# Kernel tuning notes

Measured on AMD Instinct MI355X. Metric: run time of the kernel, lower is better.

Reference implementation:

```python
import jax, jax.numpy as jnp
import numpy as np

LOSS_W = 0.6
UNC_W = 0.4
EPS = 1e-8


def setup_inputs() -> dict:
    key = jax.random.key(0)
    ks = jax.random.split(key, 6)
    B, D, C, BANK = 1024, 256, 80, 65536
    return {
        "features": jax.random.normal(ks[0], (B, D), jnp.float32),
        "predictions": jax.random.normal(ks[1], (B, C), jnp.float32),
        "targets": jax.random.uniform(ks[2], (B, C), dtype=jnp.float32),
        "query": jax.random.normal(ks[3], (B, D), jnp.float32),
        "memory": jax.random.normal(ks[4], (BANK, D), jnp.float32),
        "importance_scores": jax.random.uniform(ks[5], (BANK,), dtype=jnp.float32),
        "index": BANK,  # bank pre-filled (steady state)
        "k": 8,
    }


def _difficulty(predictions, targets):
    # per-sample BCE-with-logits, mean over classes
    bce = -(targets * jax.nn.log_sigmoid(predictions)
            + (1.0 - targets) * jax.nn.log_sigmoid(-predictions))
    sl = bce.mean(axis=1)                                   # [B]
    mx = sl.max()
    sl = jnp.where(mx > 0, sl / (mx + EPS), sl)
    probs = jax.nn.sigmoid(predictions)
    confidence = jnp.abs(probs - 0.5).mean(axis=1)
    uncertainty = jnp.clip(1.0 - 2.0 * confidence, 0.0, 1.0)
    return LOSS_W * sl + UNC_W * uncertainty                # [B]


def _update(memory, importance_scores, index, features, difficulty):
    # 'hard' mode: store samples above the 0.7 difficulty quantile,
    # sequential priority (min-replacement) insertion via scan.
    bank_size = memory.shape[0]
    thr = jnp.quantile(difficulty, 0.7)
    store = difficulty > thr                                # [B] bool

    def step(carry, inp):
        mem, scores, idx = carry
        feat, score, st = inp
        fill = idx < bank_size
        min_idx = jnp.argmin(scores)
        min_score = scores[min_idx]
        widx = jnp.where(fill, idx, min_idx)
        do_write = st & (fill | (score > min_score))
        mem = mem.at[widx].set(jnp.where(do_write, feat, mem[widx]))
        scores = scores.at[widx].set(jnp.where(do_write, score, scores[widx]))
        idx = idx + jnp.where(st & fill, 1, 0).astype(idx.dtype)
        return (mem, scores, idx), None

    init = (memory, importance_scores, jnp.asarray(index, jnp.int32))
    (mem, scores, idx), _ = jax.lax.scan(step, init, (features, difficulty, store))
    return mem, scores, idx


def _l2norm(x):
    # torch F.normalize: x / max(||x||, eps)
    n = jnp.linalg.norm(x, axis=1, keepdims=True)
    return x / jnp.maximum(n, 1e-12)


def reference(features, predictions, targets, query, memory, importance_scores, index, k):
    difficulty = _difficulty(predictions, targets)
    mem, scores, idx = _update(memory, importance_scores, index, features, difficulty)
    # retrieve: bank is full (index starts at bank_size) -> valid_size == bank_size
    sim = _l2norm(query) @ _l2norm(mem).T                   # [B, BANK]
    w, ind = jax.lax.top_k(sim, k)                          # [B, k]
    weights = jax.nn.softmax(w, axis=1)                     # [B, k]
    gathered = mem[ind]                                     # [B, k, D]
    return jnp.einsum('bk,bkd->bd', weights, gathered)      # [B, D]
```

## Files before the change

kernel.cpp:

```cpp
#include <hip/hip_runtime.h>
#include <hip/hip_bf16.h>
#include <stdint.h>

#define BANK 65536
#define BQ 1024
#define DIM 256
#define NCLS 80
#define KTOP 8
#define CAND_CAP 1024
#define SCORE_CUT 0.007f
#define NSPLIT 128
#define SPLIT_ROWS 512
#define NT 16
#define TAU 0.2f
#define SCAP 96

typedef __attribute__((ext_vector_type(8))) short short8;
typedef __attribute__((ext_vector_type(4))) float f32x4;

__device__ __forceinline__ unsigned int mono_f32(float f) {
    unsigned int b = __float_as_uint(f);
    return (b & 0x80000000u) ? ~b : (b | 0x80000000u);
}
__device__ __forceinline__ float unmono_f32(unsigned int u) {
    unsigned int b = (u & 0x80000000u) ? (u & 0x7FFFFFFFu) : ~u;
    return __uint_as_float(b);
}
__device__ __forceinline__ unsigned short f2bf(float f) {
    unsigned int u = __float_as_uint(f);
    unsigned int r = ((u >> 16) & 1u) + 0x7FFFu;
    return (unsigned short)((u + r) >> 16);
}
__device__ __forceinline__ void stage16(const char* gsrc, char* ldst) {
    __builtin_amdgcn_global_load_lds(
        (const __attribute__((address_space(1))) unsigned int*)gsrc,
        (__attribute__((address_space(3))) unsigned int*)ldst, 16, 0, 0);
}

#define INS8(L, key) do { \
    _Pragma("unroll") \
    for (int pp = 7; pp >= 1; --pp) { \
        unsigned long long prev = L[pp - 1]; \
        L[pp] = (L[pp] >= (key)) ? L[pp] : ((prev >= (key)) ? (key) : prev); \
    } \
    L[0] = (L[0] >= (key)) ? L[0] : (key); \
} while (0)

__global__ void prep_all(const float* __restrict__ memory, const float* __restrict__ features,
                         const float* __restrict__ query,
                         const float* __restrict__ pred, const float* __restrict__ targ,
                         const float* __restrict__ scores,
                         unsigned short* __restrict__ Mn, unsigned short* __restrict__ Qn,
                         float* __restrict__ invm, float* __restrict__ invq,
                         float* __restrict__ sl_raw, float* __restrict__ unc,
                         int* __restrict__ ovw, unsigned long long* __restrict__ cand,
                         int* __restrict__ meta) {
    int bx = blockIdx.x;
    if (bx < 16640) {
        int wid = threadIdx.x >> 6, lane = threadIdx.x & 63;
        int row = bx * 4 + wid;
        bool isq = (row >= BANK);
        const float* src = isq ? (query + (size_t)(row - BANK) * DIM)
                               : (memory + (size_t)row * DIM);
        float4 v = *(const float4*)(src + lane * 4);
        float ss = v.x * v.x + v.y * v.y + v.z * v.z + v.w * v.w;
        for (int off = 32; off; off >>= 1) ss += __shfl_xor(ss, off);
        float inv = 1.f / fmaxf(sqrtf(ss), 1e-12f);
        ushort4 o;
        o.x = f2bf(v.x * inv); o.y = f2bf(v.y * inv);
        o.z = f2bf(v.z * inv); o.w = f2bf(v.w * inv);
        if (!isq) {
            *(ushort4*)(Mn + (size_t)row * DIM + lane * 4) = o;
            if (lane == 0) invm[row] = inv;
        } else {
            *(ushort4*)(Qn + (size_t)(row - BANK) * DIM + lane * 4) = o;
            if (lane == 0) invq[row - BANK] = inv;
        }
    } else if (bx < 16896) {
        int wid = threadIdx.x >> 6, lane = threadIdx.x & 63;
        int b = (bx - 16640) * 4 + wid;
        float bce = 0.f, conf = 0.f;
        for (int c = lane; c < NCLS; c += 64) {
            float x = pred[b * NCLS + c];
            float t = targ[b * NCLS + c];
            float l1 = log1pf(expf(-fabsf(x)));
            float sp_pos = fmaxf(x, 0.f) + l1;
            float sp_neg = fmaxf(-x, 0.f) + l1;
            bce += t * sp_neg + (1.f - t) * sp_pos;
            float p = 1.f / (1.f + expf(-x));
            conf += fabsf(p - 0.5f);
        }
        for (int off = 32; off; off >>= 1) {
            bce += __shfl_xor(bce, off);
            conf += __shfl_xor(conf, off);
        }
        if (lane == 0) {
            sl_raw[b] = bce / (float)NCLS;
            float u = 1.f - 2.f * (conf / (float)NCLS);
            unc[b] = fminf(fmaxf(u, 0.f), 1.f);
        }
    } else {
        int i = (bx - 16896) * 256 + threadIdx.x;
        ovw[i] = -1;
        float s = scores[i];
        if (s < SCORE_CUT) {
            int pos = atomicAdd(&meta[1], 1);
            if (pos < CAND_CAP)
                cand[pos] = ((unsigned long long)__float_as_uint(s) << 32) | (unsigned long long)(unsigned)i;
        }
    }
}

__global__ void select_scatter(const float* __restrict__ sl_raw, const float* __restrict__ unc,
                               const unsigned long long* __restrict__ cand,
                               int* __restrict__ meta, int* __restrict__ ovw,
                               int* __restrict__ wlist) {
    __shared__ float red[BQ];
    __shared__ int hist[1024];
    __shared__ int pfx[1024];
    __shared__ int p[BQ];
    __shared__ int sidx[BQ];
    __shared__ int fill[1024];
    __shared__ unsigned long long kc[CAND_CAP];
    __shared__ unsigned long long buck[CAND_CAP];
    __shared__ float binvals[128];
    __shared__ int bincnt;
    __shared__ int b716s, b717s;
    __shared__ float q716s, q717s;
    int tid = threadIdx.x;

    float sl = sl_raw[tid];
    float u = unc[tid];
    red[tid] = sl;
    hist[tid] = 0;
    __syncthreads();
    for (int off = 512; off; off >>= 1) {
        if (tid < off) red[tid] = fmaxf(red[tid], red[tid + off]);
        __syncthreads();
    }
    float mx = red[0];
    float sln = (mx > 0.f) ? sl / (mx + 1e-8f) : sl;
    float diff = 0.6f * sln + 0.4f * u;
    int mybin = (int)(diff * 1024.f);
    mybin = (mybin < 0) ? 0 : ((mybin > 1023) ? 1023 : mybin);
    atomicAdd(&hist[mybin], 1);
    __syncthreads();
    pfx[tid] = hist[tid];
    __syncthreads();
    for (int off = 1; off < 1024; off <<= 1) {
        int t = (tid >= off) ? pfx[tid - off] : 0;
        __syncthreads();
        pfx[tid] += t;
        __syncthreads();
    }
    int pe = pfx[tid] - hist[tid];
    if (pe <= 716 && 716 < pfx[tid]) b716s = tid;
    if (pe <= 717 && 717 < pfx[tid]) b717s = tid;
    __syncthreads();
#pragma unroll
    for (int pass = 0; pass < 2; ++pass) {
        int target = 716 + pass;
        if (tid == 0) bincnt = 0;
        __syncthreads();
        int tb = (pass == 0) ? b716s : b717s;
        if (mybin == tb) {
            int pos = atomicAdd(&bincnt, 1);
            if (pos < 128) binvals[pos] = diff;
        }
        __syncthreads();
        if (tid == 0) {
            int bc = bincnt; if (bc > 128) bc = 128;
            for (int i = 1; i < bc; ++i) {
                float v = binvals[i]; int j = i - 1;
                while (j >= 0 && binvals[j] > v) { binvals[j + 1] = binvals[j]; --j; }
                binvals[j + 1] = v;
            }
            int base = pfx[tb] - hist[tb];
            float val = binvals[target - base];
            if (pass == 0) q716s = val; else q717s = val;
        }
        __syncthreads();
    }
    float qpos = 0.7f * (float)(BQ - 1);
    float g = qpos - floorf(qpos);
    float thr = q716s + g * (q717s - q716s);
    int flag = (diff > thr) ? 1 : 0;
    p[tid] = flag;
    __syncthreads();
    for (int off = 1; off < BQ; off <<= 1) {
        int t = (tid >= off) ? p[tid - off] : 0;
        __syncthreads();
        p[tid] += t;
        __syncthreads();
    }
    if (flag) sidx[p[tid] - 1] = tid;
    __syncthreads();
    int m = p[BQ - 1];

    int n = meta[1];
    if (n > CAND_CAP) n = CAND_CAP;
    if (m > n) m = n;
    if (tid == 0) meta[2] = m;
    kc[tid] = (tid < n) ? cand[tid] : 0xFFFFFFFFFFFFFFFFull;
    hist[tid] = 0;
    fill[tid] = 0;
    __syncthreads();
    int mybin2 = 0;
    if (tid < n) {
        float s = __uint_as_float((unsigned)(kc[tid] >> 32));
        mybin2 = (int)(s * (1024.f / SCORE_CUT));
        mybin2 = (mybin2 < 0) ? 0 : ((mybin2 > 1023) ? 1023 : mybin2);
        atomicAdd(&hist[mybin2], 1);
    }
    __syncthreads();
    pfx[tid] = hist[tid];
    __syncthreads();
    for (int off = 1; off < 1024; off <<= 1) {
        int t = (tid >= off) ? pfx[tid - off] : 0;
        __syncthreads();
        pfx[tid] += t;
        __syncthreads();
    }
    if (tid < n) {
        int pe2 = pfx[mybin2] - hist[mybin2];
        int slot = pe2 + atomicAdd(&fill[mybin2], 1);
        buck[slot] = kc[tid];
    }
    __syncthreads();
    if (tid < n) {
        int pe2 = pfx[mybin2] - hist[mybin2];
        int cnt2 = hist[mybin2];
        unsigned long long me = kc[tid];
        int rank = pe2;
        for (int i = 0; i < cnt2; ++i) rank += (buck[pe2 + i] < me) ? 1 : 0;
        if (rank < m) {
            int row = (int)(unsigned)(me & 0xFFFFFFFFu);
            ovw[row] = sidx[rank];
            wlist[rank] = row;
        }
    }
}

__global__ void patch_kernel(const float* __restrict__ features, const int* __restrict__ ovw,
                             const int* __restrict__ wlist, const int* __restrict__ meta,
                             unsigned short* __restrict__ Mn, float* __restrict__ invm) {
    int wid = threadIdx.x >> 6, lane = threadIdx.x & 63;
    int j = blockIdx.x * 4 + wid;
    if (j >= meta[2]) return;
    int row = wlist[j];
    int s = ovw[row];
    const float* src = features + (size_t)s * DIM;
    float4 v = *(const float4*)(src + lane * 4);
    float ss = v.x * v.x + v.y * v.y + v.z * v.z + v.w * v.w;
    for (int off = 32; off; off >>= 1) ss += __shfl_xor(ss, off);
    float inv = 1.f / fmaxf(sqrtf(ss), 1e-12f);
    ushort4 o;
    o.x = f2bf(v.x * inv); o.y = f2bf(v.y * inv);
    o.z = f2bf(v.z * inv); o.w = f2bf(v.w * inv);
    *(ushort4*)(Mn + (size_t)row * DIM + lane * 4) = o;
    if (lane == 0) invm[row] = inv;
}

__global__ __launch_bounds__(256, 4) void sim_coarse(
    const unsigned short* __restrict__ Qn, const unsigned short* __restrict__ Mn,
    int* __restrict__ surv, int* __restrict__ cnt) {
    __shared__ char smem[2 * 16384];

    int bx = blockIdx.x;
    int qt = bx >> 7;
    int split = bx & 127;
    int tid = threadIdx.x;
    int lane = tid & 63;
    int w = tid >> 6;
    int le = lane & 15;
    int lg = lane >> 4;
    int qbase = qt * 128 + w * 32;
    int r0 = split * SPLIT_ROWS;
    int rot = (lg + 4 * (le & 7)) & 31;

    short8 qf[2][8];
#pragma unroll
    for (int qg = 0; qg < 2; ++qg)
#pragma unroll
        for (int ks = 0; ks < 8; ++ks)
            qf[qg][ks] = *(const short8*)((const char*)Qn +
                (size_t)(qbase + qg * 16 + le) * 512 + ks * 64 + lg * 16);

#define STAGE_TILE(tidx, bufbase) do { \
    int _rr0 = r0 + (tidx) * 32; \
    _Pragma("unroll") \
    for (int _i = 0; _i < 4; ++_i) { \
        int _p = _i * 4096 + tid * 16; \
        int _row = _p >> 9; \
        int _pc = (_p >> 4) & 31; \
        int _lc = (_pc - 4 * (_row & 7)) & 31; \
        const char* _g = (const char*)Mn + (size_t)(_rr0 + _row) * 512 + _lc * 16; \
        stage16(_g, smem + (bufbase) + _p); \
    } \
} while (0)

    STAGE_TILE(0, 0);

    for (int t = 0; t < NT; ++t) {
        int cur = (t & 1) * 16384;
        __syncthreads();
        if (t + 1 < NT) STAGE_TILE(t + 1, 16384 - cur);

        f32x4 acc[2][2];
#pragma unroll
        for (int rg = 0; rg < 2; ++rg)
#pragma unroll
            for (int qg = 0; qg < 2; ++qg)
                acc[rg][qg] = (f32x4){0.f, 0.f, 0.f, 0.f};

#pragma unroll
        for (int ks = 0; ks < 8; ++ks) {
            int colb = ((ks * 4 + rot) & 31) << 4;
#pragma unroll
            for (int rg = 0; rg < 2; ++rg) {
                short8 af = *(const short8*)(smem + cur + (rg * 16 + le) * 512 + colb);
#pragma unroll
                for (int qg = 0; qg < 2; ++qg)
                    acc[rg][qg] = __builtin_amdgcn_mfma_f32_16x16x32_bf16(af, qf[qg][ks], acc[rg][qg], 0, 0, 0);
            }
        }

        int rbase = r0 + t * 32 + lg * 4;
#pragma unroll
        for (int rg = 0; rg < 2; ++rg) {
            int rb = rbase + rg * 16;
#pragma unroll
            for (int qg = 0; qg < 2; ++qg) {
                f32x4 a = acc[rg][qg];
                float gmax = fmaxf(fmaxf(a[0], a[1]), fmaxf(a[2], a[3]));
                if (gmax >= TAU) {
                    int q = qbase + qg * 16 + le;
#pragma unroll
                    for (int j = 0; j < 4; ++j) {
                        if (a[j] >= TAU) {
                            int pos = atomicAdd(&cnt[q], 1);
                            if (pos < SCAP) surv[q * SCAP + pos] = rb + j;
                        }
                    }
                }
            }
        }
    }
}

__global__ void rerank(const int* __restrict__ surv, const int* __restrict__ cnt,
                       const float* __restrict__ query, const float* __restrict__ features,
                       const float* __restrict__ memory, const int* __restrict__ ovw,
                       const float* __restrict__ invq, const float* __restrict__ invm,
                       float* __restrict__ out) {
    __shared__ int crow[SCAP];
    __shared__ float cval[SCAP];
    __shared__ float w8[KTOP];
    __shared__ int r8[KTOP];
    int q = blockIdx.x;
    int tid = threadIdx.x;
    int n = cnt[q]; if (n > SCAP) n = SCAP;
    for (int i = tid; i < SCAP; i += 256) crow[i] = (i < n) ? surv[q * SCAP + i] : 0;
    __syncthreads();
    int wv = tid >> 6, lane = tid & 63;
    float4 qv = *(const float4*)(query + (size_t)q * DIM + lane * 4);
    float iq = invq[q];
    for (int j0 = 0; j0 < n; j0 += 32) {
        for (int jj = 0; jj < 8; ++jj) {
            int j = j0 + wv * 8 + jj;
            if (j < n) {
                int r = crow[j];
                int s = ovw[r];
                const float* src = (s >= 0) ? (features + (size_t)s * DIM) : (memory + (size_t)r * DIM);
                float4 mv = *(const float4*)(src + lane * 4);
                float d = qv.x * mv.x + qv.y * mv.y + qv.z * mv.z + qv.w * mv.w;
                for (int off = 32; off; off >>= 1) d += __shfl_xor(d, off);
                if (lane == 0) cval[j] = d * iq * invm[r];
            }
        }
    }
    __syncthreads();
    if (tid == 0) {
        unsigned long long t8[8];
#pragma unroll
        for (int j = 0; j < 8; ++j) t8[j] = 0ull;
        for (int j = 0; j < n; ++j) {
            unsigned long long key =
                ((unsigned long long)mono_f32(cval[j]) << 32) |
                (unsigned long long)(0xFFFFFFFFu - (unsigned)crow[j]);
            if (key > t8[7]) INS8(t8, key);
        }
        float s[KTOP], e[KTOP];
        float sum = 0.f;
#pragma unroll
        for (int j = 0; j < KTOP; ++j) {
            s[j] = unmono_f32((unsigned)(t8[j] >> 32));
            int r = (int)(0xFFFFFFFFu - (unsigned)(t8[j] & 0xFFFFFFFFu));
            r8[j] = (r < 0) ? 0 : ((r >= BANK) ? 0 : r);
        }
        float mx = s[0];
#pragma unroll
        for (int j = 0; j < KTOP; ++j) { e[j] = expf(s[j] - mx); sum += e[j]; }
#pragma unroll
        for (int j = 0; j < KTOP; ++j) w8[j] = e[j] / sum;
    }
    __syncthreads();
    int d = tid;
    float accv = 0.f;
#pragma unroll
    for (int j = 0; j < KTOP; ++j) {
        int r = r8[j];
        int s2 = ovw[r];
        const float* src = (s2 >= 0) ? (features + (size_t)s2 * DIM) : (memory + (size_t)r * DIM);
        accv = fmaf(w8[j], src[d], accv);
    }
    out[(size_t)q * DIM + d] = accv;
}

extern "C" void kernel_launch(void* const* d_in, const int* in_sizes, int n_in,
                              void* d_out, int out_size, void* d_ws, size_t ws_size,
                              hipStream_t stream) {
    const float* features = (const float*)d_in[0];
    const float* predictions = (const float*)d_in[1];
    const float* targets = (const float*)d_in[2];
    const float* query = (const float*)d_in[3];
    const float* memory = (const float*)d_in[4];
    const float* scores = (const float*)d_in[5];
    float* out = (float*)d_out;

    char* ws = (char*)d_ws;
    int* cnt = (int*)(ws);
    int* meta = (int*)(ws + 4096);
    float* sl_raw = (float*)(ws + 8192);
    float* unc = (float*)(ws + 12288);
    int* wlist = (int*)(ws + 16384);
    float* invq = (float*)(ws + 20480);
    unsigned long long* cand = (unsigned long long*)(ws + 24576);
    int* surv = (int*)(ws + 32768);
    int* ovw = (int*)(ws + 425984);
    float* invm = (float*)(ws + 688128);
    unsigned short* Qn = (unsigned short*)(ws + 1048576);
    unsigned short* Mn = (unsigned short*)(ws + 2097152);

    hipMemsetAsync(ws, 0, 8192, stream);
    prep_all<<<17152, 256, 0, stream>>>(memory, features, query, predictions, targets, scores,
                                        Mn, Qn, invm, invq, sl_raw, unc, ovw, cand, meta);
    select_scatter<<<1, BQ, 0, stream>>>(sl_raw, unc, cand, meta, ovw, wlist);
    patch_kernel<<<256, 256, 0, stream>>>(features, ovw, wlist, meta, Mn, invm);
    sim_coarse<<<8 * NSPLIT, 256, 0, stream>>>(Qn, Mn, surv, cnt);
    rerank<<<BQ, 256, 0, stream>>>(surv, cnt, query, features, memory, ovw, invq, invm, out);
}
```

Measured before the change: 121.2 us.

## Deepen sim_coarse staging to 4-buffer ring and regroup rerank dot products

The coarse similarity kernel now stages 16-row tiles into a four-slot shared-memory ring with three tiles in flight. It waits with explicit vmcnt counts and a raw s_barrier instead of __syncthreads, aiming to overlap global loads with MFMA work more deeply. The rerank kernel now computes each candidate dot product with a 16-lane group instead of a full 64-lane wave, so more candidates are processed in parallel with fewer shuffle steps. The risk is that the hand-written vmcnt values must match the number of outstanding loads per stage, and each tile now does less MFMA work between barriers.

```diff
diff --git a/kernel.cpp b/kernel.cpp
--- a/kernel.cpp
+++ b/kernel.cpp
@@ -11,7 +11,7 @@
 #define SCORE_CUT 0.007f
 #define NSPLIT 128
 #define SPLIT_ROWS 512
-#define NT 16
+#define NT 32
 #define TAU 0.2f
 #define SCAP 96
 
@@ -264,7 +264,7 @@
 __global__ __launch_bounds__(256, 4) void sim_coarse(
     const unsigned short* __restrict__ Qn, const unsigned short* __restrict__ Mn,
     int* __restrict__ surv, int* __restrict__ cnt) {
-    __shared__ char smem[2 * 16384];
+    __shared__ char smem[4 * 8192];
 
     int bx = blockIdx.x;
     int qt = bx >> 7;
@@ -287,9 +287,9 @@
                 (size_t)(qbase + qg * 16 + le) * 512 + ks * 64 + lg * 16);
 
 #define STAGE_TILE(tidx, bufbase) do { \
-    int _rr0 = r0 + (tidx) * 32; \
+    int _rr0 = r0 + (tidx) * 16; \
     _Pragma("unroll") \
-    for (int _i = 0; _i < 4; ++_i) { \
+    for (int _i = 0; _i < 2; ++_i) { \
         int _p = _i * 4096 + tid * 16; \
         int _row = _p >> 9; \
         int _pc = (_p >> 4) & 31; \
@@ -300,47 +300,46 @@
 } while (0)
 
     STAGE_TILE(0, 0);
+    STAGE_TILE(1, 8192);
+    STAGE_TILE(2, 16384);
 
     for (int t = 0; t < NT; ++t) {
-        int cur = (t & 1) * 16384;
-        __syncthreads();
-        if (t + 1 < NT) STAGE_TILE(t + 1, 16384 - cur);
-
-        f32x4 acc[2][2];
-#pragma unroll
-        for (int rg = 0; rg < 2; ++rg)
-#pragma unroll
-            for (int qg = 0; qg < 2; ++qg)
-                acc[rg][qg] = (f32x4){0.f, 0.f, 0.f, 0.f};
+        if (t < NT - 2) {
+            asm volatile("s_waitcnt vmcnt(4)" ::: "memory");
+        } else if (t == NT - 2) {
+            asm volatile("s_waitcnt vmcnt(2)" ::: "memory");
+        } else {
+            asm volatile("s_waitcnt vmcnt(0)" ::: "memory");
+        }
+        __builtin_amdgcn_s_barrier();
+        __builtin_amdgcn_sched_barrier(0);
+        if (t + 3 < NT) STAGE_TILE(t + 3, ((t + 3) & 3) * 8192);
+        const char* base = smem + (t & 3) * 8192;
+
+        f32x4 acc[2];
+#pragma unroll
+        for (int qg = 0; qg < 2; ++qg) acc[qg] = (f32x4){0.f, 0.f, 0.f, 0.f};
 
 #pragma unroll
         for (int ks = 0; ks < 8; ++ks) {
             int colb = ((ks * 4 + rot) & 31) << 4;
-#pragma unroll
-            for (int rg = 0; rg < 2; ++rg) {
-                short8 af = *(const short8*)(smem + cur + (rg * 16 + le) * 512 + colb);
-#pragma unroll
-                for (int qg = 0; qg < 2; ++qg)
-                    acc[rg][qg] = __builtin_amdgcn_mfma_f32_16x16x32_bf16(af, qf[qg][ks], acc[rg][qg], 0, 0, 0);
-            }
-        }
-
-        int rbase = r0 + t * 32 + lg * 4;
-#pragma unroll
-        for (int rg = 0; rg < 2; ++rg) {
-            int rb = rbase + rg * 16;
-#pragma unroll
-            for (int qg = 0; qg < 2; ++qg) {
-                f32x4 a = acc[rg][qg];
-                float gmax = fmaxf(fmaxf(a[0], a[1]), fmaxf(a[2], a[3]));
-                if (gmax >= TAU) {
-                    int q = qbase + qg * 16 + le;
-#pragma unroll
-                    for (int j = 0; j < 4; ++j) {
-                        if (a[j] >= TAU) {
-                            int pos = atomicAdd(&cnt[q], 1);
-                            if (pos < SCAP) surv[q * SCAP + pos] = rb + j;
-                        }
+            short8 af = *(const short8*)(base + le * 512 + colb);
+            acc[0] = __builtin_amdgcn_mfma_f32_16x16x32_bf16(af, qf[0][ks], acc[0], 0, 0, 0);
+            acc[1] = __builtin_amdgcn_mfma_f32_16x16x32_bf16(af, qf[1][ks], acc[1], 0, 0, 0);
+        }
+
+        int rb = r0 + t * 16 + lg * 4;
+#pragma unroll
+        for (int qg = 0; qg < 2; ++qg) {
+            f32x4 a = acc[qg];
+            float gmax = fmaxf(fmaxf(a[0], a[1]), fmaxf(a[2], a[3]));
+            if (gmax >= TAU) {
+                int q = qbase + qg * 16 + le;
+#pragma unroll
+                for (int j = 0; j < 4; ++j) {
+                    if (a[j] >= TAU) {
+                        int pos = atomicAdd(&cnt[q], 1);
+                        if (pos < SCAP) surv[q * SCAP + pos] = rb + j;
                     }
                 }
             }
@@ -362,22 +361,28 @@
     int n = cnt[q]; if (n > SCAP) n = SCAP;
     for (int i = tid; i < SCAP; i += 256) crow[i] = (i < n) ? surv[q * SCAP + i] : 0;
     __syncthreads();
-    int wv = tid >> 6, lane = tid & 63;
-    float4 qv = *(const float4*)(query + (size_t)q * DIM + lane * 4);
+    int grp = tid >> 4;
+    int l16 = tid & 15;
+    float4 qv4[4];
+#pragma unroll
+    for (int k = 0; k < 4; ++k)
+        qv4[k] = *(const float4*)(query + (size_t)q * DIM + l16 * 16 + k * 4);
     float iq = invq[q];
-    for (int j0 = 0; j0 < n; j0 += 32) {
-        for (int jj = 0; jj < 8; ++jj) {
-            int j = j0 + wv * 8 + jj;
-            if (j < n) {
-                int r = crow[j];
-                int s = ovw[r];
-                const float* src = (s >= 0) ? (features + (size_t)s * DIM) : (memory + (size_t)r * DIM);
-                float4 mv = *(const float4*)(src + lane * 4);
-                float d = qv.x * mv.x + qv.y * mv.y + qv.z * mv.z + qv.w * mv.w;
-                for (int off = 32; off; off >>= 1) d += __shfl_xor(d, off);
-                if (lane == 0) cval[j] = d * iq * invm[r];
-            }
-        }
+    for (int j = grp; j < n; j += 16) {
+        int r = crow[j];
+        int s = ovw[r];
+        const float* src = (s >= 0) ? (features + (size_t)s * DIM) : (memory + (size_t)r * DIM);
+        float d = 0.f;
+#pragma unroll
+        for (int k = 0; k < 4; ++k) {
+            float4 mv = *(const float4*)(src + l16 * 16 + k * 4);
+            d += qv4[k].x * mv.x + qv4[k].y * mv.y + qv4[k].z * mv.z + qv4[k].w * mv.w;
+        }
+        d += __shfl_xor(d, 1);
+        d += __shfl_xor(d, 2);
+        d += __shfl_xor(d, 4);
+        d += __shfl_xor(d, 8);
+        if (l16 == 0) cval[j] = d * iq * invm[r];
     }
     __syncthreads();
     if (tid == 0) {
```

Result: no change. 120.0 us (-1.0%).
